# Performance work log

Measured on AMD Instinct MI355X. Metric: run time of the kernel, lower is better.

Reference implementation:

```python
import jax, jax.numpy as jnp
import numpy as np

EPS = 1e-08

def setup_inputs() -> dict:
    key = jax.random.key(0)
    k1, = jax.random.split(key, 1)
    B, C, H, W = 8, 128, 128, 256
    inp = jax.random.normal(k1, (B, C, H, W), dtype=jnp.float32)
    gain = jnp.ones((1, C, 1, 1), dtype=jnp.float32)
    bias = jnp.zeros((1, C, 1, 1), dtype=jnp.float32)
    return {"inp": inp, "gain": gain, "bias": bias}

def reference(inp, gain, bias):
    # LayerNorm over the last dim (W), then per-channel affine.
    # (Original torch code computes mean/var via a Python loop of adds;
    #  the intended math is a plain last-dim mean/variance.)
    mean = jnp.mean(inp, axis=-1, keepdims=True)
    centered = inp - mean
    var = jnp.mean(centered * centered, axis=-1, keepdims=True)
    std = jnp.sqrt(var + EPS)
    x = centered / std
    return x * gain + bias
```

## Files before the change

### kernel.cpp

```cpp
#include <hip/hip_runtime.h>


#define W_DIM 256
#define C_DIM 128
#define EPS 1e-8f

typedef float f32x4 __attribute__((ext_vector_type(4)));

__global__ __launch_bounds__(256) void tLNv3_kernel(
    const float* __restrict__ inp,
    const float* __restrict__ gain,
    const float* __restrict__ bias,
    float* __restrict__ out,
    const int rows, const int wave_stride)
{
    const int lane = threadIdx.x & 63;
    int row = (int)(blockIdx.x << 2) + (threadIdx.x >> 6);
    if (row >= rows) return;

    const f32x4* __restrict__ in4  = (const f32x4*)inp;
    f32x4* __restrict__       out4 = (f32x4*)out;

    f32x4 v = in4[(size_t)row * 64 + lane];

    for (;;) {
        const int  nrow      = row + wave_stride;
        const bool have_next = (nrow < rows);
        f32x4 vn = {};
        if (have_next) vn = in4[(size_t)nrow * 64 + lane];

        float s  = v.x + v.y + v.z + v.w;
        float sq = v.x * v.x + v.y * v.y + v.z * v.z + v.w * v.w;

        #pragma unroll
        for (int off = 1; off < 64; off <<= 1) {
            s  += __shfl_xor(s,  off, 64);
            sq += __shfl_xor(sq, off, 64);
        }

        const float mean = s * (1.0f / (float)W_DIM);
        const float var  = sq * (1.0f / (float)W_DIM) - mean * mean;
        const float rstd = rsqrtf(var + EPS);

        const int   c = (row >> 7) & (C_DIM - 1);
        const float g = gain[c];
        const float b = bias[c];

        f32x4 o;
        o.x = (v.x - mean) * rstd * g + b;
        o.y = (v.y - mean) * rstd * g + b;
        o.z = (v.z - mean) * rstd * g + b;
        o.w = (v.w - mean) * rstd * g + b;
        out4[(size_t)row * 64 + lane] = o;

        if (!have_next) break;
        v   = vn;
        row = nrow;
    }
}

extern "C" void kernel_launch(void* const* d_in, const int* in_sizes, int n_in,
                              void* d_out, int out_size, void* d_ws, size_t ws_size,
                              hipStream_t stream)
{
    const float* inp  = (const float*)d_in[0];
    const float* gain = (const float*)d_in[1];
    const float* bias = (const float*)d_in[2];
    float* out = (float*)d_out;

    const int rows = in_sizes[0] / W_DIM;

    int blocks = (rows + 3) / 4;
    if (blocks > 2048) blocks = 2048;
    const int wave_stride = blocks * 4;

    tLNv3_kernel<<<blocks, 256, 0, stream>>>(inp, gain, bias, out, rows, wave_stride);
}
```

Baseline: 233.6 us.

## Process eight rows per wave with 16-lane row groups and nontemporal stores

Each wave now covers eight rows. Each group of 16 lanes owns a row and issues eight independent vector loads up front, replacing the grid-stride loop that prefetched one row at a time. The row reduction needs only four shuffle steps. The normalize-plus-affine is folded into a single FMA per element. Outputs are written with nontemporal stores, and the grid is launched with one wave per eight rows. This is meant to raise memory-level parallelism on a bandwidth-bound kernel, at the cost of more registers per thread and a bounds check only on the first row of each pair.

```diff
diff --git a/kernel.cpp b/kernel.cpp
--- a/kernel.cpp
+++ b/kernel.cpp
@@ -7,56 +7,85 @@
 
 typedef float f32x4 __attribute__((ext_vector_type(4)));
 
-__global__ __launch_bounds__(256) void tLNv3_kernel(
+__device__ __forceinline__ void accum(const f32x4 v, float& s, float& q)
+{
+    s += (v.x + v.y) + (v.z + v.w);
+    q = fmaf(v.x, v.x, q); q = fmaf(v.y, v.y, q);
+    q = fmaf(v.z, v.z, q); q = fmaf(v.w, v.w, q);
+}
+
+__device__ __forceinline__ f32x4 affine(const f32x4 v, const float a, const float bb)
+{
+    f32x4 o;
+    o.x = fmaf(v.x, a, bb); o.y = fmaf(v.y, a, bb);
+    o.z = fmaf(v.z, a, bb); o.w = fmaf(v.w, a, bb);
+    return o;
+}
+
+__global__ __launch_bounds__(256) void tLNv5_kernel(
     const float* __restrict__ inp,
     const float* __restrict__ gain,
     const float* __restrict__ bias,
     float* __restrict__ out,
-    const int rows, const int wave_stride)
+    const int rows)
 {
     const int lane = threadIdx.x & 63;
-    int row = (int)(blockIdx.x << 2) + (threadIdx.x >> 6);
-    if (row >= rows) return;
+    const int sub  = lane & 15;
+    const int quad = lane >> 4;
+    const int gw   = (int)(blockIdx.x << 2) + (threadIdx.x >> 6);
+
+    const int r0 = (gw << 3) + quad;
+    if (r0 >= rows) return;
 
     const f32x4* __restrict__ in4  = (const f32x4*)inp;
     f32x4* __restrict__       out4 = (f32x4*)out;
 
-    f32x4 v = in4[(size_t)row * 64 + lane];
+    const size_t b0 = (size_t)r0 * 64 + sub;
+    const size_t b1 = b0 + 256;
 
-    for (;;) {
-        const int  nrow      = row + wave_stride;
-        const bool have_next = (nrow < rows);
-        f32x4 vn = {};
-        if (have_next) vn = in4[(size_t)nrow * 64 + lane];
+    f32x4 a0 = in4[b0];
+    f32x4 a1 = in4[b0 + 16];
+    f32x4 a2 = in4[b0 + 32];
+    f32x4 a3 = in4[b0 + 48];
+    f32x4 c0 = in4[b1];
+    f32x4 c1 = in4[b1 + 16];
+    f32x4 c2 = in4[b1 + 32];
+    f32x4 c3 = in4[b1 + 48];
 
-        float s  = v.x + v.y + v.z + v.w;
-        float sq = v.x * v.x + v.y * v.y + v.z * v.z + v.w * v.w;
+    float sA = 0.f, qA = 0.f, sB = 0.f, qB = 0.f;
+    accum(a0, sA, qA); accum(a1, sA, qA); accum(a2, sA, qA); accum(a3, sA, qA);
+    accum(c0, sB, qB); accum(c1, sB, qB); accum(c2, sB, qB); accum(c3, sB, qB);
 
-        #pragma unroll
-        for (int off = 1; off < 64; off <<= 1) {
-            s  += __shfl_xor(s,  off, 64);
-            sq += __shfl_xor(sq, off, 64);
-        }
+    #pragma unroll
+    for (int off = 1; off < 16; off <<= 1) {
+        sA += __shfl_xor(sA, off, 64);
+        qA += __shfl_xor(qA, off, 64);
+        sB += __shfl_xor(sB, off, 64);
+        qB += __shfl_xor(qB, off, 64);
+    }
 
-        const float mean = s * (1.0f / (float)W_DIM);
-        const float var  = sq * (1.0f / (float)W_DIM) - mean * mean;
-        const float rstd = rsqrtf(var + EPS);
+    const int   ch = (r0 >> 7) & (C_DIM - 1);
+    const float g  = gain[ch];
+    const float bv = bias[ch];
 
-        const int   c = (row >> 7) & (C_DIM - 1);
-        const float g = gain[c];
-        const float b = bias[c];
+    const float meanA = sA * (1.0f / (float)W_DIM);
+    const float varA  = qA * (1.0f / (float)W_DIM) - meanA * meanA;
+    const float aA    = rsqrtf(varA + EPS) * g;
+    const float bbA   = bv - meanA * aA;
 
-        f32x4 o;
-        o.x = (v.x - mean) * rstd * g + b;
-        o.y = (v.y - mean) * rstd * g + b;
-        o.z = (v.z - mean) * rstd * g + b;
-        o.w = (v.w - mean) * rstd * g + b;
-        out4[(size_t)row * 64 + lane] = o;
+    const float meanB = sB * (1.0f / (float)W_DIM);
+    const float varB  = qB * (1.0f / (float)W_DIM) - meanB * meanB;
+    const float aB    = rsqrtf(varB + EPS) * g;
+    const float bbB   = bv - meanB * aB;
 
-        if (!have_next) break;
-        v   = vn;
-        row = nrow;
-    }
+    __builtin_nontemporal_store(affine(a0, aA, bbA), &out4[b0]);
+    __builtin_nontemporal_store(affine(a1, aA, bbA), &out4[b0 + 16]);
+    __builtin_nontemporal_store(affine(a2, aA, bbA), &out4[b0 + 32]);
+    __builtin_nontemporal_store(affine(a3, aA, bbA), &out4[b0 + 48]);
+    __builtin_nontemporal_store(affine(c0, aB, bbB), &out4[b1]);
+    __builtin_nontemporal_store(affine(c1, aB, bbB), &out4[b1 + 16]);
+    __builtin_nontemporal_store(affine(c2, aB, bbB), &out4[b1 + 32]);
+    __builtin_nontemporal_store(affine(c3, aB, bbB), &out4[b1 + 48]);
 }
 
 extern "C" void kernel_launch(void* const* d_in, const int* in_sizes, int n_in,
@@ -68,11 +97,9 @@
     const float* bias = (const float*)d_in[2];
     float* out = (float*)d_out;
 
-    const int rows = in_sizes[0] / W_DIM;
+    const int rows   = in_sizes[0] / W_DIM;
+    const int waves  = (rows + 7) / 8;
+    const int blocks = (waves + 3) / 4;
 
-    int blocks = (rows + 3) / 4;
-    if (blocks > 2048) blocks = 2048;
-    const int wave_stride = blocks * 4;
-
-    tLNv3_kernel<<<blocks, 256, 0, stream>>>(inp, gain, bias, out, rows, wave_stride);
+    tLNv5_kernel<<<blocks, 256, 0, stream>>>(inp, gain, bias, out, rows);
 }
```

Result: no change. 234.7 us (+0.5%).

## Deepen row prefetch to four in flight with nontemporal stores

Applied to the files above, without the earlier changes.

Adds a fast path for the exact row count of the test shape (8192 waves times 16 rows) in which each wave keeps four row loads in flight, unrolls all sixteen rows, and precomputes the two channel gain/bias pairs it needs. The affine step is folded into one FMA per element, and the output is written with nontemporal stores to avoid polluting cache. The goal is more memory-level parallelism for a bandwidth-bound kernel. A generic fallback loop handles any other row count, and the extra live registers may reduce occupancy.

```diff
diff --git a/kernel.cpp b/kernel.cpp
--- a/kernel.cpp
+++ b/kernel.cpp
@@ -7,55 +7,97 @@
 
 typedef float f32x4 __attribute__((ext_vector_type(4)));
 
-__global__ __launch_bounds__(256) void tLNv3_kernel(
+#define NWAVES 8192
+#define RPW    16
+
+__global__ __launch_bounds__(256) void tLNv6_kernel(
     const float* __restrict__ inp,
     const float* __restrict__ gain,
     const float* __restrict__ bias,
     float* __restrict__ out,
-    const int rows, const int wave_stride)
+    const int rows)
 {
     const int lane = threadIdx.x & 63;
-    int row = (int)(blockIdx.x << 2) + (threadIdx.x >> 6);
-    if (row >= rows) return;
+    const int gw   = (int)(blockIdx.x << 2) + (threadIdx.x >> 6);
 
     const f32x4* __restrict__ in4  = (const f32x4*)inp;
     f32x4* __restrict__       out4 = (f32x4*)out;
 
-    f32x4 v = in4[(size_t)row * 64 + lane];
+    if (rows == NWAVES * RPW) {
+        const size_t base = (size_t)gw * 64 + lane;
+        const size_t STEP = (size_t)NWAVES * 64;
 
-    for (;;) {
-        const int  nrow      = row + wave_stride;
-        const bool have_next = (nrow < rows);
-        f32x4 vn = {};
-        if (have_next) vn = in4[(size_t)nrow * 64 + lane];
+        const int   c0 = (gw >> 7) & (C_DIM - 1);
+        const int   c1 = (c0 + 64) & (C_DIM - 1);
+        const float g0 = gain[c0], b0 = bias[c0];
+        const float g1 = gain[c1], b1 = bias[c1];
 
-        float s  = v.x + v.y + v.z + v.w;
-        float sq = v.x * v.x + v.y * v.y + v.z * v.z + v.w * v.w;
+        f32x4 s0 = in4[base];
+        f32x4 s1 = in4[base + STEP];
+        f32x4 s2 = in4[base + 2 * STEP];
+        f32x4 s3 = in4[base + 3 * STEP];
 
-        #pragma unroll
-        for (int off = 1; off < 64; off <<= 1) {
-            s  += __shfl_xor(s,  off, 64);
-            sq += __shfl_xor(sq, off, 64);
+        #define LN_STEP(k, s, gg, bb_)                                         \
+        {                                                                      \
+            float sum = (s.x + s.y) + (s.z + s.w);                             \
+            float sq  = s.x * s.x;                                             \
+            sq = fmaf(s.y, s.y, sq); sq = fmaf(s.z, s.z, sq);                  \
+            sq = fmaf(s.w, s.w, sq);                                           \
+            _Pragma("unroll")                                                  \
+            for (int off = 1; off < 64; off <<= 1) {                           \
+                sum += __shfl_xor(sum, off, 64);                               \
+                sq  += __shfl_xor(sq,  off, 64);                               \
+            }                                                                  \
+            const float mean = sum * (1.0f / (float)W_DIM);                    \
+            const float var  = sq * (1.0f / (float)W_DIM) - mean * mean;       \
+            const float a    = rsqrtf(var + EPS) * gg;                         \
+            const float bb   = bb_ - mean * a;                                 \
+            f32x4 o;                                                           \
+            o.x = fmaf(s.x, a, bb); o.y = fmaf(s.y, a, bb);                    \
+            o.z = fmaf(s.z, a, bb); o.w = fmaf(s.w, a, bb);                    \
+            if ((k) + 4 < RPW) s = in4[base + ((size_t)((k) + 4)) * STEP];     \
+            __builtin_nontemporal_store(o, &out4[base + ((size_t)(k)) * STEP]);\
         }
 
-        const float mean = s * (1.0f / (float)W_DIM);
-        const float var  = sq * (1.0f / (float)W_DIM) - mean * mean;
-        const float rstd = rsqrtf(var + EPS);
-
-        const int   c = (row >> 7) & (C_DIM - 1);
-        const float g = gain[c];
-        const float b = bias[c];
-
-        f32x4 o;
-        o.x = (v.x - mean) * rstd * g + b;
-        o.y = (v.y - mean) * rstd * g + b;
-        o.z = (v.z - mean) * rstd * g + b;
-        o.w = (v.w - mean) * rstd * g + b;
-        out4[(size_t)row * 64 + lane] = o;
-
-        if (!have_next) break;
-        v   = vn;
-        row = nrow;
+        LN_STEP(0,  s0, g0, b0)
+        LN_STEP(1,  s1, g1, b1)
+        LN_STEP(2,  s2, g0, b0)
+        LN_STEP(3,  s3, g1, b1)
+        LN_STEP(4,  s0, g0, b0)
+        LN_STEP(5,  s1, g1, b1)
+        LN_STEP(6,  s2, g0, b0)
+        LN_STEP(7,  s3, g1, b1)
+        LN_STEP(8,  s0, g0, b0)
+        LN_STEP(9,  s1, g1, b1)
+        LN_STEP(10, s2, g0, b0)
+        LN_STEP(11, s3, g1, b1)
+        LN_STEP(12, s0, g0, b0)
+        LN_STEP(13, s1, g1, b1)
+        LN_STEP(14, s2, g0, b0)
+        LN_STEP(15, s3, g1, b1)
+        #undef LN_STEP
+    } else {
+        for (int row = gw; row < rows; row += NWAVES) {
+            f32x4 v = in4[(size_t)row * 64 + lane];
+            float sum = (v.x + v.y) + (v.z + v.w);
+            float sq  = v.x * v.x;
+            sq = fmaf(v.y, v.y, sq); sq = fmaf(v.z, v.z, sq);
+            sq = fmaf(v.w, v.w, sq);
+            #pragma unroll
+            for (int off = 1; off < 64; off <<= 1) {
+                sum += __shfl_xor(sum, off, 64);
+                sq  += __shfl_xor(sq,  off, 64);
+            }
+            const float mean = sum * (1.0f / (float)W_DIM);
+            const float var  = sq * (1.0f / (float)W_DIM) - mean * mean;
+            const int   c    = (row >> 7) & (C_DIM - 1);
+            const float a    = rsqrtf(var + EPS) * gain[c];
+            const float bb   = bias[c] - mean * a;
+            f32x4 o;
+            o.x = fmaf(v.x, a, bb); o.y = fmaf(v.y, a, bb);
+            o.z = fmaf(v.z, a, bb); o.w = fmaf(v.w, a, bb);
+            out4[(size_t)row * 64 + lane] = o;
+        }
     }
 }
 
@@ -68,11 +110,8 @@
     const float* bias = (const float*)d_in[2];
     float* out = (float*)d_out;
 
-    const int rows = in_sizes[0] / W_DIM;
+    const int rows   = in_sizes[0] / W_DIM;
+    const int blocks = NWAVES / 4;
 
-    int blocks = (rows + 3) / 4;
-    if (blocks > 2048) blocks = 2048;
-    const int wave_stride = blocks * 4;
-
-    tLNv3_kernel<<<blocks, 256, 0, stream>>>(inp, gain, bias, out, rows, wave_stride);
+    tLNv6_kernel<<<blocks, 256, 0, stream>>>(inp, gain, bias, out, rows);
 }
```

New measurement: 236.9 us. No clear change (+1.4%).

## Use one row per wave with DPP reductions and folded affine

Applied to the files above, without the earlier changes.

Drops the grid-stride persistent loop with software prefetch and launches one wave per row across the full grid. Replaces the shuffle-xor butterfly reductions with DPP row shifts and row broadcasts plus a readlane of lane 63. Folds mean, rstd, gain and bias into a single scale and offset so each output is one fma. This trades latency hiding through prefetch for more waves in flight, and cuts the cross-lane reduction cost on a memory-bound kernel.

```diff
diff --git a/kernel.cpp b/kernel.cpp
--- a/kernel.cpp
+++ b/kernel.cpp
@@ -7,56 +7,61 @@
 
 typedef float f32x4 __attribute__((ext_vector_type(4)));
 
-__global__ __launch_bounds__(256) void tLNv3_kernel(
+template <int CTRL>
+__device__ __forceinline__ float dpp_add(float x)
+{
+    int moved = __builtin_amdgcn_update_dpp(
+        0, __builtin_bit_cast(int, x), CTRL, 0xf, 0xf, true);
+    return x + __builtin_bit_cast(float, moved);
+}
+
+__device__ __forceinline__ float read_lane63(float x)
+{
+    return __builtin_bit_cast(
+        float, __builtin_amdgcn_readlane(__builtin_bit_cast(int, x), 63));
+}
+
+__global__ __launch_bounds__(256) void tLNv7_kernel(
     const float* __restrict__ inp,
     const float* __restrict__ gain,
     const float* __restrict__ bias,
     float* __restrict__ out,
-    const int rows, const int wave_stride)
+    const int rows)
 {
     const int lane = threadIdx.x & 63;
-    int row = (int)(blockIdx.x << 2) + (threadIdx.x >> 6);
+    const int row  = (int)(blockIdx.x << 2) + (threadIdx.x >> 6);
     if (row >= rows) return;
 
     const f32x4* __restrict__ in4  = (const f32x4*)inp;
     f32x4* __restrict__       out4 = (f32x4*)out;
 
-    f32x4 v = in4[(size_t)row * 64 + lane];
+    const size_t base = (size_t)row * 64 + lane;
+    const f32x4 v = in4[base];
 
-    for (;;) {
-        const int  nrow      = row + wave_stride;
-        const bool have_next = (nrow < rows);
-        f32x4 vn = {};
-        if (have_next) vn = in4[(size_t)nrow * 64 + lane];
+    float s = (v.x + v.y) + (v.z + v.w);
+    float q = v.x * v.x;
+    q = fmaf(v.y, v.y, q); q = fmaf(v.z, v.z, q); q = fmaf(v.w, v.w, q);
 
-        float s  = v.x + v.y + v.z + v.w;
-        float sq = v.x * v.x + v.y * v.y + v.z * v.z + v.w * v.w;
+    s = dpp_add<0x111>(s); q = dpp_add<0x111>(q);
+    s = dpp_add<0x112>(s); q = dpp_add<0x112>(q);
+    s = dpp_add<0x114>(s); q = dpp_add<0x114>(q);
+    s = dpp_add<0x118>(s); q = dpp_add<0x118>(q);
+    s = dpp_add<0x142>(s); q = dpp_add<0x142>(q);
+    s = dpp_add<0x143>(s); q = dpp_add<0x143>(q);
+    const float sum = read_lane63(s);
+    const float sq  = read_lane63(q);
 
-        #pragma unroll
-        for (int off = 1; off < 64; off <<= 1) {
-            s  += __shfl_xor(s,  off, 64);
-            sq += __shfl_xor(sq, off, 64);
-        }
+    const float mean = sum * (1.0f / (float)W_DIM);
+    const float var  = sq  * (1.0f / (float)W_DIM) - mean * mean;
 
-        const float mean = s * (1.0f / (float)W_DIM);
-        const float var  = sq * (1.0f / (float)W_DIM) - mean * mean;
-        const float rstd = rsqrtf(var + EPS);
+    const int   c = (row >> 7) & (C_DIM - 1);
+    const float a  = rsqrtf(var + EPS) * gain[c];
+    const float bb = bias[c] - mean * a;
 
-        const int   c = (row >> 7) & (C_DIM - 1);
-        const float g = gain[c];
-        const float b = bias[c];
-
-        f32x4 o;
-        o.x = (v.x - mean) * rstd * g + b;
-        o.y = (v.y - mean) * rstd * g + b;
-        o.z = (v.z - mean) * rstd * g + b;
-        o.w = (v.w - mean) * rstd * g + b;
-        out4[(size_t)row * 64 + lane] = o;
-
-        if (!have_next) break;
-        v   = vn;
-        row = nrow;
-    }
+    f32x4 o;
+    o.x = fmaf(v.x, a, bb); o.y = fmaf(v.y, a, bb);
+    o.z = fmaf(v.z, a, bb); o.w = fmaf(v.w, a, bb);
+    out4[base] = o;
 }
 
 extern "C" void kernel_launch(void* const* d_in, const int* in_sizes, int n_in,
@@ -68,11 +73,8 @@
     const float* bias = (const float*)d_in[2];
     float* out = (float*)d_out;
 
-    const int rows = in_sizes[0] / W_DIM;
+    const int rows   = in_sizes[0] / W_DIM;
+    const int blocks = (rows + 3) / 4;
 
-    int blocks = (rows + 3) / 4;
-    if (blocks > 2048) blocks = 2048;
-    const int wave_stride = blocks * 4;
-
-    tLNv3_kernel<<<blocks, 256, 0, stream>>>(inp, gain, bias, out, rows, wave_stride);
+    tLNv7_kernel<<<blocks, 256, 0, stream>>>(inp, gain, bias, out, rows);
 }
```

Result: faster. 221.7 us (-5.1%).
